# Performance work log

Hardware: AMD Instinct MI355X
Metric: run time of the kernel (lower is better)

Reference implementation:

```python
import jax, jax.numpy as jnp
import numpy as np

STRIDE = 16
NUM_A = 9
POS_TH, NEG_TH = 0.7, 0.3
FG, BG, IGN = 1.0, 0.0, 2.0
CAP = 128  # BATCH_SIZE * 0.5 for both fg and bg


def _generate_base_anchors(base_size=16, ratios=(0.5, 1.0, 2.0), scales=(8, 16, 32)):
    w = h = float(base_size)
    xc = yc = 0.5 * (base_size - 1)
    size = w * h
    out = []
    for r in ratios:
        ws = np.round(np.sqrt(size / r))
        hs = np.round(ws * r)
        for s in scales:
            W, H = ws * s, hs * s
            out.append([xc - 0.5 * (W - 1), yc - 0.5 * (H - 1),
                        xc + 0.5 * (W - 1), yc + 0.5 * (H - 1)])
    return np.asarray(out, dtype=np.float32)  # [9,4]


def _all_anchors(H, W):
    base = _generate_base_anchors()
    sx = np.arange(W, dtype=np.float32) * STRIDE
    sy = np.arange(H, dtype=np.float32) * STRIDE
    xs, ys = np.meshgrid(sx, sy)  # row-major over (h, w)
    shifts = np.stack([xs.ravel(), ys.ravel(), xs.ravel(), ys.ravel()], 1)
    return jnp.asarray((shifts[:, None, :] + base[None, :, :]).reshape(-1, 4))  # [H*W*9,4], order (h,w,a)


def _forward(scores, gt, im_w, im_h):
    H, W = scores.shape[2], scores.shape[3]
    anchors = _all_anchors(H, W)  # [N,4]
    valid = (anchors[:, 0] >= 0.) & (anchors[:, 1] >= 0.) & \
            (anchors[:, 2] < im_w) & (anchors[:, 3] < im_h)
    # pairwise IoU with +1 box convention
    aw = anchors[:, 2] - anchors[:, 0] + 1.
    ah = anchors[:, 3] - anchors[:, 1] + 1.
    a_area = jnp.where((aw > 0) & (ah > 0), aw * ah, 0.)
    gw = gt[:, 2] - gt[:, 0] + 1.
    gh = gt[:, 3] - gt[:, 1] + 1.
    g_area = jnp.where((gw > 0) & (gh > 0), gw * gh, 0.)
    ix1 = jnp.maximum(anchors[:, None, 0], gt[None, :, 0])
    iy1 = jnp.maximum(anchors[:, None, 1], gt[None, :, 1])
    ix2 = jnp.minimum(anchors[:, None, 2], gt[None, :, 2])
    iy2 = jnp.minimum(anchors[:, None, 3], gt[None, :, 3])
    iw = ix2 - ix1 + 1.
    ih = iy2 - iy1 + 1.
    inter = jnp.where((iw > 0) & (ih > 0), iw * ih, 0.)
    ovl = inter / (a_area[:, None] + g_area[None, :] - inter)  # [N,G]
    ovl_m = jnp.where(valid[:, None], ovl, -1.)  # exclude invalid anchors
    a_argmax = jnp.argmax(ovl, axis=1)           # best gt per anchor
    a_max = jnp.max(ovl, axis=1)
    g_max = jnp.max(ovl_m, axis=0)               # best (valid) anchor overlap per gt
    gt_fg = jnp.any(ovl_m == g_max[None, :], axis=1) & valid
    labels = jnp.where(valid & (a_max < NEG_TH), BG, IGN)
    labels = jnp.where(gt_fg, FG, labels)
    labels = jnp.where(valid & (a_max >= POS_TH), FG, labels)
    # random subsample fg/bg down to CAP each (matches npr.choice semantics in distribution)
    kf, kb = jax.random.split(jax.random.key(42))
    def subsample(lbl, mask, k):
        s = jnp.where(mask, jax.random.uniform(k, lbl.shape), jnp.inf)
        ranks = jnp.argsort(jnp.argsort(s))
        keep = ranks < jnp.minimum(jnp.sum(mask), CAP)
        return jnp.where(mask & ~keep, IGN, lbl)
    labels = subsample(labels, labels == FG, kf)
    labels = subsample(labels, labels == BG, kb)
    num_ni = jnp.sum(labels != IGN).astype(jnp.float32)
    gts = gt[a_argmax]
    ax = (anchors[:, 2] + anchors[:, 0]) * 0.5
    ay = (anchors[:, 3] + anchors[:, 1]) * 0.5
    gwm = gts[:, 2] - gts[:, 0] + 1.
    ghm = gts[:, 3] - gts[:, 1] + 1.
    gx = (gts[:, 2] + gts[:, 0]) * 0.5
    gy = (gts[:, 3] + gts[:, 1]) * 0.5
    adj = jnp.stack([(gx - ax) / aw, (gy - ay) / ah,
                     jnp.log(gwm / aw), jnp.log(ghm / ah)], axis=1)  # [N,4]
    adj = jnp.where(valid[:, None], adj, 0.)
    wts = jnp.where((labels == FG)[:, None], 1.0 / num_ni, 0.) * jnp.ones((1, 4), jnp.float32)
    labels_out = labels.reshape(1, H, W, NUM_A).transpose(0, 3, 1, 2) \
                       .reshape(1, 1, NUM_A * H, W).astype(jnp.int32)
    adj_out = adj.reshape(1, H, W, 4 * NUM_A).transpose(0, 3, 1, 2)
    wts_out = wts.reshape(1, H, W, 4 * NUM_A).transpose(0, 3, 1, 2)
    return labels_out, adj_out, wts_out


def setup_inputs() -> dict:
    key = jax.random.key(0)
    k1, k2, k3 = jax.random.split(key, 3)
    scores = jax.random.normal(k1, (1, 18, 256, 256), dtype=jnp.float32)
    G = 64
    cxy = jax.random.uniform(k2, (G, 2), minval=100., maxval=3900.)
    wh = jax.random.uniform(k3, (G, 2), minval=32., maxval=512.)
    x1y1 = jnp.clip(cxy - wh * 0.5, 0., 4095.)
    x2y2 = jnp.clip(cxy + wh * 0.5, 0., 4095.)
    gt = jnp.concatenate([x1y1, x2y2], axis=1)  # [G,4] = x1,y1,x2,y2
    return {"anchor_object_scores": scores, "ground_truth_boxes": gt,
            "im_w": 4096, "im_h": 4096}


def reference(anchor_object_scores, ground_truth_boxes, im_w, im_h):
    return _forward(anchor_object_scores, ground_truth_boxes, im_w, im_h)
```

## Files before the change

kernel.cpp:

```cpp
#include <hip/hip_runtime.h>
#include <stdint.h>


#define NUM_A 9
#define HW 65536
#define N_ANCH 589824
#define NG 64
#define CAPK 128u
#define NBINS 256
#define BG_TC 65536u
#define CAND_CAP 2048

#define LAB_BG 0u
#define LAB_FG 1u
#define LAB_IGN 2u

#define NBLK 1152
#define NGRP 64
#define GQ 18

#define OFF_HF    0
#define OFF_HB    256
#define OFF_TOTF  512
#define OFF_TOTB  1536
#define OFF_SUBB  2560
#define OFF_ROOTB 3584
#define OFF_SUBD  3600
#define OFF_ROOTD 4624
#define OFF_SEL   4640
#define OFF_CFLG  4656
#define OFF_CNTF  5680
#define OFF_CNTB  5696
#define CTRL_WORDS 5712
#define OFF_ZFLG  CTRL_WORDS
#define OFF_CANDF (OFF_ZFLG + 64*16)
#define OFF_CANDB (OFF_CANDF + 2*CAND_CAP)

#define MAGIC_C 0x5CA1AB1Eu
#define MAGIC_Z 0x7A3F19C5u

__constant__ float BA[NUM_A][4] = {
  { -84.f,  -40.f,  99.f,  55.f}, {-176.f,  -88.f, 191.f, 103.f},
  {-360.f, -184.f, 375.f, 199.f}, { -56.f,  -56.f,  71.f,  71.f},
  {-120.f, -120.f, 135.f, 135.f}, {-248.f, -248.f, 263.f, 263.f},
  { -36.f,  -80.f,  51.f,  95.f}, { -80.f, -168.f,  95.f, 183.f},
  {-168.f, -344.f, 183.f, 359.f}};

__host__ __device__ static inline void tf2x32(uint32_t k0, uint32_t k1,
                                              uint32_t x0, uint32_t x1,
                                              uint32_t* o0, uint32_t* o1) {
  const uint32_t ks2 = k0 ^ k1 ^ 0x1BD11BDAu;
#define TF_R(r) { x0 += x1; x1 = (x1 << (r)) | (x1 >> (32 - (r))); x1 ^= x0; }
  x0 += k0; x1 += k1;
  TF_R(13) TF_R(15) TF_R(26) TF_R(6)
  x0 += k1;  x1 += ks2 + 1u;
  TF_R(17) TF_R(29) TF_R(16) TF_R(24)
  x0 += ks2; x1 += k0 + 2u;
  TF_R(13) TF_R(15) TF_R(26) TF_R(6)
  x0 += k0;  x1 += k1 + 3u;
  TF_R(17) TF_R(29) TF_R(16) TF_R(24)
  x0 += k1;  x1 += ks2 + 4u;
  TF_R(13) TF_R(15) TF_R(26) TF_R(6)
  x0 += ks2; x1 += k0 + 5u;
#undef TF_R
  *o0 = x0; *o1 = x1;
}

__device__ static inline uint32_t mant_of(uint32_t k0, uint32_t k1, uint32_t n) {
  uint32_t o0, o1;
  tf2x32(k0, k1, 0u, n, &o0, &o1);
  return (o0 ^ o1) >> 9;
}

__device__ static inline float axis_best(float blo, float bhi, float glo,
                                         float ghi, int lo, int hi) {
  #pragma clang fp contract(off)
  float t1 = (ghi - bhi) * 0.0625f;
  float t2 = (glo - blo) * 0.0625f;
  float tmin = fminf(t1, t2), tmax = fmaxf(t1, t2);
  int c1 = (int)floorf(tmin), c2 = (int)ceilf(tmax);
  int cand0 = lo, cand1 = hi;
  int cand2 = min(max(c1,     lo), hi);
  int cand3 = min(max(c1 + 1, lo), hi);
  int cand4 = min(max(c2 - 1, lo), hi);
  int cand5 = min(max(c2,     lo), hi);
  float best = -3.0e38f;
  int cands[6] = {cand0, cand1, cand2, cand3, cand4, cand5};
  #pragma unroll
  for (int i = 0; i < 6; i++) {
    float s = (float)(cands[i] << 4);
    float v = fminf(bhi + s, ghi) - fmaxf(blo + s, glo) + 1.0f;
    best = fmaxf(best, v);
  }
  return best;
}

#define AG_LOAD(p)      __hip_atomic_load((p), __ATOMIC_RELAXED, __HIP_MEMORY_SCOPE_AGENT)
#define AG_STORE(p, v)  __hip_atomic_store((p), (v), __ATOMIC_RELAXED, __HIP_MEMORY_SCOPE_AGENT)

__global__ __launch_bounds__(256) void k_one(const float* __restrict__ gt,
                                             const int* __restrict__ imw_p,
                                             const int* __restrict__ imh_p,
                                             float* __restrict__ out_lab,
                                             float* __restrict__ out_adj,
                                             float* __restrict__ out_wts,
                                             uint32_t* __restrict__ ws,
                                             uint32_t kf0, uint32_t kf1,
                                             uint32_t kb0, uint32_t kb1) {
  #pragma clang fp contract(off)
  __shared__ uint64_t scB[CAND_CAP];
  uint32_t* sh = (uint32_t*)scB;
  __shared__ float sg0[NG], sg1[NG], sg2[NG], sg3[NG], sga[NG], sgm[NG];
  __shared__ uint32_t sgmU[NG];
  __shared__ unsigned long long sMask[4];
  __shared__ int sAnyZero, sLastB, sLastD;
  __shared__ uint32_t sSel[10];
  __shared__ uint32_t sCF, sCB;
  int tid = threadIdx.x;
  int b = blockIdx.x;
  int a = b >> 7, hb = (b & 127) << 1;
  int grp = b & (NGRP - 1);

  if (b == 0) {
    for (int i = tid; i < CTRL_WORDS; i += 256) AG_STORE(&ws[i], 0u);
    asm volatile("s_waitcnt vmcnt(0)" ::: "memory");
    __syncthreads();
    if (tid < NGRP) AG_STORE(&ws[OFF_ZFLG + tid * 16], MAGIC_Z);
  }

  ((uint2*)sh)[tid] = make_uint2(0, 0);
  if (tid == 0) { sAnyZero = 0; sCF = 0u; sCB = 0u; }
  if (tid < NG) {
    const float4 g4 = ((const float4*)gt)[tid];
    sg0[tid] = g4.x; sg1[tid] = g4.y; sg2[tid] = g4.z; sg3[tid] = g4.w;
    float gw = g4.z - g4.x + 1.0f, gh = g4.w - g4.y + 1.0f;
    sga[tid] = (gw > 0.0f && gh > 0.0f) ? gw * gh : 0.0f;
    sgmU[tid] = 0u;
  }
  __syncthreads();

  {
    int imwi = imw_p[0], imhi = imh_p[0];
    for (int p = tid; p < NG * NUM_A; p += 256) {
      int g = p / NUM_A, q = p - g * NUM_A;
      float b0 = BA[q][0], b1 = BA[q][1], b2 = BA[q][2], b3 = BA[q][3];
      int ib0 = (int)b0, ib1 = (int)b1, ib2 = (int)b2, ib3 = (int)b3;
      int wlo = max(0, (-ib0 + 15) >> 4);
      int whi = min(255, (imwi - ib2 - 1) >> 4);
      int hlo = max(0, (-ib1 + 15) >> 4);
      int hhi = min(255, (imhi - ib3 - 1) >> 4);
      if (wlo > whi || hlo > hhi) continue;
      float iwb = axis_best(b0, b2, sg0[g], sg2[g], wlo, whi);
      float ihb = axis_best(b1, b3, sg1[g], sg3[g], hlo, hhi);
      float aw = b2 - b0 + 1.0f, ah = b3 - b1 + 1.0f;
      float aarea = aw * ah;
      float inter = (iwb > 0.0f && ihb > 0.0f) ? iwb * ihb : 0.0f;
      float den = aarea + sga[g] - inter;
      float o = inter / den;
      atomicMax(&sgmU[g], __float_as_uint(o));
    }
  }

  {
    int wv = tid >> 6, g = tid & 63;
    float sy = (float)((hb + wv) << 4);
    float ihp = fminf(BA[a][3] + sy, sg3[g]) - fmaxf(BA[a][1] + sy, sg1[g]) + 1.0f;
    unsigned long long mk = __ballot(ihp > 0.0f);
    if (g == 0) sMask[wv] = mk;
  }
  __syncthreads();
  if (tid < NG) {
    uint32_t mm = sgmU[tid];
    sgm[tid] = __uint_as_float(mm);
    if (mm == 0u) atomicOr(&sAnyZero, 1);
  }
  __syncthreads();

  float BA0 = BA[a][0], BA1 = BA[a][1], BA2 = BA[a][2], BA3 = BA[a][3];
  float imw = (float)imw_p[0], imh = (float)imh_p[0];
  int w = tid;
  float sx = (float)(w << 4);
  float A0 = BA0 + sx, A2 = BA2 + sx;
  float aw = A2 - A0 + 1.0f;
  float A1v[2], A3v[2];
  #pragma unroll
  for (int r = 0; r < 2; r++) {
    float sy = (float)((hb + r) << 4);
    A1v[r] = BA1 + sy; A3v[r] = BA3 + sy;
  }
  float ah = A3v[0] - A1v[0] + 1.0f;
  float aarea = aw * ah;
  bool xv = (A0 >= 0.0f) && (A2 < imw);

  unsigned long long mk0 = sMask[0], mk1 = sMask[1];
  unsigned long long uni = mk0 | mk1;
  float amaxv[2] = {0.f, 0.f};
  int bgv[2] = {0, 0};
  uint32_t afv = 0u;
  while (uni) {
    int g = __ffsll(uni) - 1;
    uni &= uni - 1;
    float iw = fminf(A2, sg2[g]) - fmaxf(A0, sg0[g]) + 1.0f;
    if (!__any(iw > 0.0f)) continue;
    if (iw > 0.0f) {
      float base = aarea + sga[g];
      float gy1 = sg1[g], gy2 = sg3[g], gm = sgm[g];
#define DO_ROW(r, mk)                                                     \
      if ((mk >> g) & 1ull) {                                             \
        float ih = fminf(A3v[r], gy2) - fmaxf(A1v[r], gy1) + 1.0f;        \
        float inter = iw * ih;                                            \
        float o = inter / (base - inter);                                 \
        if (o > amaxv[r]) { amaxv[r] = o; bgv[r] = g; }                   \
        if (o == gm) afv |= (1u << r);                                    \
      }
      DO_ROW(0, mk0) DO_ROW(1, mk1)
#undef DO_ROW
    }
  }

  bool anyZ = (sAnyZero != 0);
  uint32_t lm[2];
  uint32_t cfLoc = 0, cbLoc = 0;
  #pragma unroll
  for (int r = 0; r < 2; r++) {
    int hw = (hb + r) * 256 + w;
    bool valid = xv && (A1v[r] >= 0.0f) && (A3v[r] < imh);
    float amax = amaxv[r];
    bool anyfg = (((afv >> r) & 1u) || anyZ) && valid;
    uint32_t lab;
    if (!valid)                       lab = LAB_IGN;
    else if (anyfg || amax >= 0.7f)   lab = LAB_FG;
    else if (amax < 0.3f)             lab = LAB_BG;
    else                              lab = LAB_IGN;

    float adj0 = 0.f, adj1 = 0.f, adj2 = 0.f, adj3 = 0.f;
    if (valid) {
      int bg = bgv[r];
      float G0 = sg0[bg], G1 = sg1[bg], G2 = sg2[bg], G3 = sg3[bg];
      float ax = (A2 + A0) * 0.5f, ay = (A3v[r] + A1v[r]) * 0.5f;
      float gwm = G2 - G0 + 1.0f, ghm = G3 - G1 + 1.0f;
      float gx = (G2 + G0) * 0.5f, gy = (G3 + G1) * 0.5f;
      adj0 = (gx - ax) / aw;
      adj1 = (gy - ay) / ah;
      adj2 = logf(gwm / aw);
      adj3 = logf(ghm / ah);
    }
    int c4 = a * 4;
    out_adj[(c4 + 0) * HW + hw] = adj0;
    out_adj[(c4 + 1) * HW + hw] = adj1;
    out_adj[(c4 + 2) * HW + hw] = adj2;
    out_adj[(c4 + 3) * HW + hw] = adj3;

    uint32_t m = 0u;
    uint32_t n = (uint32_t)(hw * 9 + a);
    if (lab != LAB_IGN) {
      uint32_t kk0 = (lab == LAB_FG) ? kf0 : kb0;
      uint32_t kk1 = (lab == LAB_FG) ? kf1 : kb1;
      m = mant_of(kk0, kk1, n);
      if (lab == LAB_FG) {
        cfLoc++;
        atomicAdd(&sh[m >> 15], 1u);
      } else {
        cbLoc++;
        if (m < BG_TC) atomicAdd(&sh[NBINS + (m >> 8)], 1u);
      }
    }
    lm[r] = (lab << 24) | m;
  }
  if (cfLoc) atomicAdd(&sCF, cfLoc);
  if (cbLoc) atomicAdd(&sCB, cbLoc);
  __syncthreads();

  if (tid == 0) {
    while (AG_LOAD(&ws[OFF_ZFLG + grp * 16]) != MAGIC_Z)
      __builtin_amdgcn_s_sleep(2);
  }
  __syncthreads();

  for (int i = tid; i < 2 * NBINS; i += 256) {
    uint32_t v = sh[i];
    if (v) atomicAdd(&ws[OFF_HF + i], v);
  }
  if (tid == 0) {
    if (sCF) atomicAdd(&ws[OFF_TOTF + grp * 16], sCF);
    if (sCB) atomicAdd(&ws[OFF_TOTB + grp * 16], sCB);
  }
  asm volatile("s_waitcnt vmcnt(0)" ::: "memory");
  __syncthreads();

  if (tid == 0) {
    int last = 0;
    uint32_t v = atomicAdd(&ws[OFF_SUBB + grp * 16], 1u);
    if (v == GQ - 1) {
      uint32_t r = atomicAdd(&ws[OFF_ROOTB], 1u);
      if (r == NGRP - 1) last = 1;
    }
    sLastB = last;
  }
  __syncthreads();
  if (sLastB) {
    __shared__ uint32_t sTots[128];
    if (tid < NGRP)            sTots[tid] = AG_LOAD(&ws[OFF_TOTF + tid * 16]);
    else if (tid < 2 * NGRP)
      sTots[tid] = AG_LOAD(&ws[OFF_TOTB + (tid - NGRP) * 16]);
    __syncthreads();
    uint32_t totF = 0, totB = 0;
    if (tid == 0) {
      for (int i = 0; i < NGRP; i++) {
        totF += sTots[i]; totB += sTots[NGRP + i];
      }
      sTots[0] = totF; sTots[1] = totB;
    }
    __syncthreads();
    totF = sTots[0]; totB = sTots[1];

    for (int cls = 0; cls < 2; cls++) {
      uint32_t* hist = ws + (cls ? OFF_HB : OFF_HF);
      uint32_t* sel = ws + OFF_SEL + cls * 5;
      uint32_t tot = cls ? totB : totF;
      uint32_t K = tot < CAPK ? tot : CAPK;
      uint32_t loc = AG_LOAD(&hist[tid]);
      sh[tid] = loc; __syncthreads();
      for (int off = 1; off < 256; off <<= 1) {
        uint32_t v = (tid >= off) ? sh[tid - off] : 0u;
        __syncthreads();
        sh[tid] += v;
        __syncthreads();
      }
      if (tid == 0) {
        uint32_t mode = (K == 0u) ? 0u : ((tot <= CAPK) ? 1u : 2u);
        AG_STORE(&sel[0], mode);
        AG_STORE(&sel[4], K);
        if (mode != 2u) {
          AG_STORE(&sel[1], 0xFFFFFFFFu); AG_STORE(&sel[2], 0u);
          AG_STORE(&sel[3], 0u);
        }
      }
      if (K > 0u && tot > CAPK) {
        uint32_t myC = sh[tid], pvC = (tid == 0) ? 0u : sh[tid - 1];
        if (myC >= K && pvC < K) {
          AG_STORE(&sel[1], (uint32_t)tid); AG_STORE(&sel[2], pvC);
          AG_STORE(&sel[3], K - pvC);
        }
      }
      __syncthreads();
    }
    asm volatile("s_waitcnt vmcnt(0)" ::: "memory");
    __syncthreads();
    if (tid < NGRP) AG_STORE(&ws[OFF_CFLG + tid * 16], MAGIC_C);
  }

  if (tid == 0) {
    while (AG_LOAD(&ws[OFF_CFLG + grp * 16]) != MAGIC_C)
      __builtin_amdgcn_s_sleep(2);
  }
  __syncthreads();
  if (tid < 10) sSel[tid] = AG_LOAD(&ws[OFF_SEL + tid]);
  __syncthreads();
  uint32_t mF = sSel[0], bbF = sSel[1];
  uint32_t mB = sSel[5], bbB = sSel[6];
  uint32_t Kf = sSel[4], Kb = sSel[9];
  float inv = 1.0f / (float)(Kf + Kb);

  #pragma unroll
  for (int r = 0; r < 2; r++) {
    int hw = (hb + r) * 256 + w;
    uint32_t lab = lm[r] >> 24;
    uint32_t m = lm[r] & 0x7FFFFFu;
    uint32_t n = (uint32_t)(hw * 9 + a);
    float outv = 2.0f, wv = 0.0f;
    bool skip = false;
    if (lab == LAB_FG) {
      if (mF == 1u) { outv = 1.0f; wv = inv; }
      else if (mF == 2u) {
        uint32_t bn = m >> 15;
        if (bn < bbF) { outv = 1.0f; wv = inv; }
        else if (bn == bbF) {
          uint32_t idx = atomicAdd(&ws[OFF_CNTF], 1u);
          if (idx < CAND_CAP) {
            AG_STORE((uint64_t*)(ws + OFF_CANDF) + idx,
                     ((uint64_t)m << 20) | (uint64_t)n);
            skip = true;
          }
        }
      }
    } else if (lab == LAB_BG) {
      if (mB == 1u) { outv = 0.0f; }
      else if (mB == 2u && m < BG_TC) {
        uint32_t bn = m >> 8;
        if (bn < bbB) { outv = 0.0f; }
        else if (bn == bbB) {
          uint32_t idx = atomicAdd(&ws[OFF_CNTB], 1u);
          if (idx < CAND_CAP) {
            AG_STORE((uint64_t*)(ws + OFF_CANDB) + idx,
                     ((uint64_t)m << 20) | (uint64_t)n);
            skip = true;
          }
        }
      }
    }
    if (!skip) {
      out_lab[a * HW + hw] = outv;
      int c4 = a * 4;
      out_wts[(c4 + 0) * HW + hw] = wv;
      out_wts[(c4 + 1) * HW + hw] = wv;
      out_wts[(c4 + 2) * HW + hw] = wv;
      out_wts[(c4 + 3) * HW + hw] = wv;
    }
  }

  asm volatile("s_waitcnt vmcnt(0)" ::: "memory");
  __syncthreads();

  if (tid == 0) {
    int last = 0;
    uint32_t v = atomicAdd(&ws[OFF_SUBD + grp * 16], 1u);
    if (v == GQ - 1) {
      uint32_t r = atomicAdd(&ws[OFF_ROOTD], 1u);
      if (r == NGRP - 1) last = 1;
    }
    sLastD = last;
  }
  __syncthreads();
  if (sLastD) {
    for (int cls = 0; cls < 2; cls++) {
      uint32_t cnt = AG_LOAD(&ws[cls == 0 ? OFF_CNTF : OFF_CNTB]);
      uint32_t C = cnt < CAND_CAP ? cnt : CAND_CAP;
      uint32_t need = AG_LOAD(&ws[OFF_SEL + cls * 5 + 3]);
      const uint64_t* cand =
          (const uint64_t*)(ws + (cls == 0 ? OFF_CANDF : OFF_CANDB));
      for (uint32_t i = tid; i < C; i += 256)
        scB[i] = AG_LOAD(&cand[i]);
      __syncthreads();
      for (uint32_t i = tid; i < C; i += 256) {
        uint64_t k = scB[i];
        uint32_t rr = 0;
        for (uint32_t j = 0; j < C; j++) rr += (scB[j] < k) ? 1u : 0u;
        bool kept = (rr < need);
        uint32_t nn = (uint32_t)(k & 0xFFFFFu);
        uint32_t aa = nn % 9u, hww = nn / 9u;
        uint32_t tt = aa * HW + hww;
        float lv = kept ? (cls == 0 ? 1.0f : 0.0f) : 2.0f;
        float wvv = (kept && cls == 0) ? inv : 0.0f;
        AG_STORE(&out_lab[tt], lv);
        #pragma unroll
        for (int j2 = 0; j2 < 4; j2++)
          AG_STORE(&out_wts[(aa * 4 + j2) * HW + hww], wvv);
      }
      __syncthreads();
    }
    if (tid < NGRP) AG_STORE(&ws[OFF_ZFLG + tid * 16], 0u);
  }
}

extern "C" void kernel_launch(void* const* d_in, const int* in_sizes, int n_in,
                              void* d_out, int out_size, void* d_ws,
                              size_t ws_size, hipStream_t stream) {
  const float* gt  = (const float*)d_in[1];
  const int*   imw = (const int*)d_in[2];
  const int*   imh = (const int*)d_in[3];
  float* out      = (float*)d_out;
  float* out_lab  = out;
  float* out_adj  = out + N_ANCH;
  float* out_wts  = out + 5 * N_ANCH;
  uint32_t* ws = (uint32_t*)d_ws;

  uint32_t kf0, kf1, kb0, kb1;
  tf2x32(0u, 42u, 0u, 0u, &kf0, &kf1);
  tf2x32(0u, 42u, 0u, 1u, &kb0, &kb1);

  hipLaunchKernelGGL(k_one, dim3(NBLK), dim3(256), 0, stream, gt, imw, imh,
                     out_lab, out_adj, out_wts, ws, kf0, kf1, kb0, kb1);
}
```

Measured before the change: 91.84 us.

## Drop second grid-wide barrier by pushing candidates to per-group lists for last block

Removes the second grid-wide wait (the CFLG flag spin) in which every block waited for the last block to publish the selection thresholds. Non-candidate anchors now write their ignore outputs early. FG and in-range BG candidates go into per-group global lists, and the final block applies the threshold and the tie-break ranking for all of them. This trades the global stall for more serial work in one block and caps each group's list at 128 entries. Candidates beyond that cap are written as ignore, which could change results if a group ever holds more.

```diff
diff --git a/kernel.cpp b/kernel.cpp
--- a/kernel.cpp
+++ b/kernel.cpp
@@ -9,7 +9,8 @@
 #define CAPK 128u
 #define NBINS 256
 #define BG_TC 65536u
-#define CAND_CAP 2048
+#define CLCAP 128u
+#define STAGE_CAP 2048u
 
 #define LAB_BG 0u
 #define LAB_FG 1u
@@ -25,18 +26,13 @@
 #define OFF_TOTB  1536
 #define OFF_SUBB  2560
 #define OFF_ROOTB 3584
-#define OFF_SUBD  3600
-#define OFF_ROOTD 4624
-#define OFF_SEL   4640
-#define OFF_CFLG  4656
-#define OFF_CNTF  5680
-#define OFF_CNTB  5696
-#define CTRL_WORDS 5712
+#define OFF_CCNTF 3600
+#define OFF_CCNTB 4624
+#define CTRL_WORDS 5648
 #define OFF_ZFLG  CTRL_WORDS
-#define OFF_CANDF (OFF_ZFLG + 64*16)
-#define OFF_CANDB (OFF_CANDF + 2*CAND_CAP)
-
-#define MAGIC_C 0x5CA1AB1Eu
+#define OFF_LISTF (OFF_ZFLG + 64*16)
+#define OFF_LISTB (OFF_LISTF + 2*NGRP*CLCAP)
+
 #define MAGIC_Z 0x7A3F19C5u
 
 __constant__ float BA[NUM_A][4] = {
@@ -108,14 +104,18 @@
                                              uint32_t kf0, uint32_t kf1,
                                              uint32_t kb0, uint32_t kb1) {
   #pragma clang fp contract(off)
-  __shared__ uint64_t scB[CAND_CAP];
+  __shared__ uint64_t scB[STAGE_CAP];
   uint32_t* sh = (uint32_t*)scB;
   __shared__ float sg0[NG], sg1[NG], sg2[NG], sg3[NG], sga[NG], sgm[NG];
   __shared__ uint32_t sgmU[NG];
   __shared__ unsigned long long sMask[4];
-  __shared__ int sAnyZero, sLastB, sLastD;
-  __shared__ uint32_t sSel[10];
+  __shared__ int sAnyZero, sLastB;
   __shared__ uint32_t sCF, sCB;
+  __shared__ uint32_t sTots[2 * NGRP];
+  __shared__ uint32_t sCnt2[NGRP];
+  __shared__ uint32_t sSelLoc[10];
+  __shared__ uint32_t sStageCnt;
+  __shared__ float sInv;
   int tid = threadIdx.x;
   int b = blockIdx.x;
   int a = b >> 7, hb = (b & 127) << 1;
@@ -266,6 +266,15 @@
       }
     }
     lm[r] = (lab << 24) | m;
+
+    bool cand = (lab == LAB_FG) || (lab == LAB_BG && m < BG_TC);
+    if (!cand) {
+      out_lab[a * HW + hw] = 2.0f;
+      out_wts[(c4 + 0) * HW + hw] = 0.0f;
+      out_wts[(c4 + 1) * HW + hw] = 0.0f;
+      out_wts[(c4 + 2) * HW + hw] = 0.0f;
+      out_wts[(c4 + 3) * HW + hw] = 0.0f;
+    }
   }
   if (cfLoc) atomicAdd(&sCF, cfLoc);
   if (cbLoc) atomicAdd(&sCB, cbLoc);
@@ -276,6 +285,31 @@
       __builtin_amdgcn_s_sleep(2);
   }
   __syncthreads();
+
+  #pragma unroll
+  for (int r = 0; r < 2; r++) {
+    uint32_t lab = lm[r] >> 24;
+    uint32_t m = lm[r] & 0x7FFFFFu;
+    bool cand = (lab == LAB_FG) || (lab == LAB_BG && m < BG_TC);
+    if (!cand) continue;
+    int hw = (hb + r) * 256 + w;
+    uint32_t n = (uint32_t)(hw * 9 + a);
+    int cls = (lab == LAB_FG) ? 0 : 1;
+    uint32_t idx = atomicAdd(
+        &ws[(cls ? OFF_CCNTB : OFF_CCNTF) + grp * 16], 1u);
+    if (idx < CLCAP) {
+      uint64_t* lst = (uint64_t*)(ws + (cls ? OFF_LISTB : OFF_LISTF)) +
+                      (uint32_t)grp * CLCAP;
+      AG_STORE(&lst[idx], ((uint64_t)m << 20) | (uint64_t)n);
+    } else {
+      out_lab[a * HW + hw] = 2.0f;
+      int c4 = a * 4;
+      out_wts[(c4 + 0) * HW + hw] = 0.0f;
+      out_wts[(c4 + 1) * HW + hw] = 0.0f;
+      out_wts[(c4 + 2) * HW + hw] = 0.0f;
+      out_wts[(c4 + 3) * HW + hw] = 0.0f;
+    }
+  }
 
   for (int i = tid; i < 2 * NBINS; i += 256) {
     uint32_t v = sh[i];
@@ -298,147 +332,89 @@
     sLastB = last;
   }
   __syncthreads();
-  if (sLastB) {
-    __shared__ uint32_t sTots[128];
-    if (tid < NGRP)            sTots[tid] = AG_LOAD(&ws[OFF_TOTF + tid * 16]);
-    else if (tid < 2 * NGRP)
-      sTots[tid] = AG_LOAD(&ws[OFF_TOTB + (tid - NGRP) * 16]);
-    __syncthreads();
+  if (!sLastB) return;
+
+  if (tid < NGRP)            sTots[tid] = AG_LOAD(&ws[OFF_TOTF + tid * 16]);
+  else if (tid < 2 * NGRP)
+    sTots[tid] = AG_LOAD(&ws[OFF_TOTB + (tid - NGRP) * 16]);
+  __syncthreads();
+  if (tid == 0) {
     uint32_t totF = 0, totB = 0;
+    for (int i = 0; i < NGRP; i++) {
+      totF += sTots[i]; totB += sTots[NGRP + i];
+    }
+    uint32_t Kf = totF < CAPK ? totF : CAPK;
+    uint32_t Kb = totB < CAPK ? totB : CAPK;
+    sTots[0] = totF; sTots[1] = totB;
+    sInv = 1.0f / (float)(Kf + Kb);
+  }
+  __syncthreads();
+  uint32_t totF = sTots[0], totB = sTots[1];
+
+  for (int cls = 0; cls < 2; cls++) {
+    uint32_t* hist = ws + (cls ? OFF_HB : OFF_HF);
+    uint32_t tot = cls ? totB : totF;
+    uint32_t K = tot < CAPK ? tot : CAPK;
+    uint32_t loc = AG_LOAD(&hist[tid]);
+    __syncthreads();
+    sh[tid] = loc; __syncthreads();
+    for (int off = 1; off < 256; off <<= 1) {
+      uint32_t v = (tid >= off) ? sh[tid - off] : 0u;
+      __syncthreads();
+      sh[tid] += v;
+      __syncthreads();
+    }
     if (tid == 0) {
-      for (int i = 0; i < NGRP; i++) {
-        totF += sTots[i]; totB += sTots[NGRP + i];
+      uint32_t mode = (K == 0u) ? 0u : ((tot <= CAPK) ? 1u : 2u);
+      sSelLoc[cls * 5 + 0] = mode;
+      sSelLoc[cls * 5 + 1] = 0xFFFFFFFFu;
+      sSelLoc[cls * 5 + 2] = 0u;
+      sSelLoc[cls * 5 + 3] = 0u;
+      sSelLoc[cls * 5 + 4] = K;
+    }
+    __syncthreads();
+    if (K > 0u && tot > CAPK) {
+      uint32_t myC = sh[tid], pvC = (tid == 0) ? 0u : sh[tid - 1];
+      if (myC >= K && pvC < K) {
+        sSelLoc[cls * 5 + 1] = (uint32_t)tid;
+        sSelLoc[cls * 5 + 2] = pvC;
+        sSelLoc[cls * 5 + 3] = K - pvC;
       }
-      sTots[0] = totF; sTots[1] = totB;
-    }
-    __syncthreads();
-    totF = sTots[0]; totB = sTots[1];
-
-    for (int cls = 0; cls < 2; cls++) {
-      uint32_t* hist = ws + (cls ? OFF_HB : OFF_HF);
-      uint32_t* sel = ws + OFF_SEL + cls * 5;
-      uint32_t tot = cls ? totB : totF;
-      uint32_t K = tot < CAPK ? tot : CAPK;
-      uint32_t loc = AG_LOAD(&hist[tid]);
-      sh[tid] = loc; __syncthreads();
-      for (int off = 1; off < 256; off <<= 1) {
-        uint32_t v = (tid >= off) ? sh[tid - off] : 0u;
-        __syncthreads();
-        sh[tid] += v;
-        __syncthreads();
-      }
-      if (tid == 0) {
-        uint32_t mode = (K == 0u) ? 0u : ((tot <= CAPK) ? 1u : 2u);
-        AG_STORE(&sel[0], mode);
-        AG_STORE(&sel[4], K);
-        if (mode != 2u) {
-          AG_STORE(&sel[1], 0xFFFFFFFFu); AG_STORE(&sel[2], 0u);
-          AG_STORE(&sel[3], 0u);
+    }
+    __syncthreads();
+  }
+  float inv = sInv;
+
+  for (int cls = 0; cls < 2; cls++) {
+    if (tid < NGRP) {
+      uint32_t c2 = AG_LOAD(&ws[(cls ? OFF_CCNTB : OFF_CCNTF) + tid * 16]);
+      sCnt2[tid] = c2 < CLCAP ? c2 : CLCAP;
+    }
+    if (tid == 0) sStageCnt = 0u;
+    __syncthreads();
+    uint32_t mode = sSelLoc[cls * 5 + 0];
+    uint32_t bb = sSelLoc[cls * 5 + 1];
+    uint32_t need = sSelLoc[cls * 5 + 3];
+    const uint64_t* lst0 =
+        (const uint64_t*)(ws + (cls ? OFF_LISTB : OFF_LISTF));
+    for (uint32_t idx = tid; idx < NGRP * CLCAP; idx += 256) {
+      uint32_t g2 = idx >> 7, i = idx & (CLCAP - 1u);
+      if (i >= sCnt2[g2]) continue;
+      uint64_t k = AG_LOAD(&lst0[g2 * CLCAP + i]);
+      uint32_t m = (uint32_t)(k >> 20);
+      uint32_t n = (uint32_t)(k & 0xFFFFFu);
+      bool decided = true, kept = false;
+      if (mode == 1u) kept = true;
+      else if (mode == 2u) {
+        uint32_t bn = cls ? (m >> 8) : (m >> 15);
+        if (bn < bb) kept = true;
+        else if (bn == bb) {
+          uint32_t s = atomicAdd(&sStageCnt, 1u);
+          if (s < STAGE_CAP) { scB[s] = k; decided = false; }
         }
       }
-      if (K > 0u && tot > CAPK) {
-        uint32_t myC = sh[tid], pvC = (tid == 0) ? 0u : sh[tid - 1];
-        if (myC >= K && pvC < K) {
-          AG_STORE(&sel[1], (uint32_t)tid); AG_STORE(&sel[2], pvC);
-          AG_STORE(&sel[3], K - pvC);
-        }
-      }
-      __syncthreads();
-    }
-    asm volatile("s_waitcnt vmcnt(0)" ::: "memory");
-    __syncthreads();
-    if (tid < NGRP) AG_STORE(&ws[OFF_CFLG + tid * 16], MAGIC_C);
-  }
-
-  if (tid == 0) {
-    while (AG_LOAD(&ws[OFF_CFLG + grp * 16]) != MAGIC_C)
-      __builtin_amdgcn_s_sleep(2);
-  }
-  __syncthreads();
-  if (tid < 10) sSel[tid] = AG_LOAD(&ws[OFF_SEL + tid]);
-  __syncthreads();
-  uint32_t mF = sSel[0], bbF = sSel[1];
-  uint32_t mB = sSel[5], bbB = sSel[6];
-  uint32_t Kf = sSel[4], Kb = sSel[9];
-  float inv = 1.0f / (float)(Kf + Kb);
-
-  #pragma unroll
-  for (int r = 0; r < 2; r++) {
-    int hw = (hb + r) * 256 + w;
-    uint32_t lab = lm[r] >> 24;
-    uint32_t m = lm[r] & 0x7FFFFFu;
-    uint32_t n = (uint32_t)(hw * 9 + a);
-    float outv = 2.0f, wv = 0.0f;
-    bool skip = false;
-    if (lab == LAB_FG) {
-      if (mF == 1u) { outv = 1.0f; wv = inv; }
-      else if (mF == 2u) {
-        uint32_t bn = m >> 15;
-        if (bn < bbF) { outv = 1.0f; wv = inv; }
-        else if (bn == bbF) {
-          uint32_t idx = atomicAdd(&ws[OFF_CNTF], 1u);
-          if (idx < CAND_CAP) {
-            AG_STORE((uint64_t*)(ws + OFF_CANDF) + idx,
-                     ((uint64_t)m << 20) | (uint64_t)n);
-            skip = true;
-          }
-        }
-      }
-    } else if (lab == LAB_BG) {
-      if (mB == 1u) { outv = 0.0f; }
-      else if (mB == 2u && m < BG_TC) {
-        uint32_t bn = m >> 8;
-        if (bn < bbB) { outv = 0.0f; }
-        else if (bn == bbB) {
-          uint32_t idx = atomicAdd(&ws[OFF_CNTB], 1u);
-          if (idx < CAND_CAP) {
-            AG_STORE((uint64_t*)(ws + OFF_CANDB) + idx,
-                     ((uint64_t)m << 20) | (uint64_t)n);
-            skip = true;
-          }
-        }
-      }
-    }
-    if (!skip) {
-      out_lab[a * HW + hw] = outv;
-      int c4 = a * 4;
-      out_wts[(c4 + 0) * HW + hw] = wv;
-      out_wts[(c4 + 1) * HW + hw] = wv;
-      out_wts[(c4 + 2) * HW + hw] = wv;
-      out_wts[(c4 + 3) * HW + hw] = wv;
-    }
-  }
-
-  asm volatile("s_waitcnt vmcnt(0)" ::: "memory");
-  __syncthreads();
-
-  if (tid == 0) {
-    int last = 0;
-    uint32_t v = atomicAdd(&ws[OFF_SUBD + grp * 16], 1u);
-    if (v == GQ - 1) {
-      uint32_t r = atomicAdd(&ws[OFF_ROOTD], 1u);
-      if (r == NGRP - 1) last = 1;
-    }
-    sLastD = last;
-  }
-  __syncthreads();
-  if (sLastD) {
-    for (int cls = 0; cls < 2; cls++) {
-      uint32_t cnt = AG_LOAD(&ws[cls == 0 ? OFF_CNTF : OFF_CNTB]);
-      uint32_t C = cnt < CAND_CAP ? cnt : CAND_CAP;
-      uint32_t need = AG_LOAD(&ws[OFF_SEL + cls * 5 + 3]);
-      const uint64_t* cand =
-          (const uint64_t*)(ws + (cls == 0 ? OFF_CANDF : OFF_CANDB));
-      for (uint32_t i = tid; i < C; i += 256)
-        scB[i] = AG_LOAD(&cand[i]);
-      __syncthreads();
-      for (uint32_t i = tid; i < C; i += 256) {
-        uint64_t k = scB[i];
-        uint32_t rr = 0;
-        for (uint32_t j = 0; j < C; j++) rr += (scB[j] < k) ? 1u : 0u;
-        bool kept = (rr < need);
-        uint32_t nn = (uint32_t)(k & 0xFFFFFu);
-        uint32_t aa = nn % 9u, hww = nn / 9u;
+      if (decided) {
+        uint32_t aa = n % 9u, hww = n / 9u;
         uint32_t tt = aa * HW + hww;
         float lv = kept ? (cls == 0 ? 1.0f : 0.0f) : 2.0f;
         float wvv = (kept && cls == 0) ? inv : 0.0f;
@@ -447,10 +423,28 @@
         for (int j2 = 0; j2 < 4; j2++)
           AG_STORE(&out_wts[(aa * 4 + j2) * HW + hww], wvv);
       }
-      __syncthreads();
-    }
-    if (tid < NGRP) AG_STORE(&ws[OFF_ZFLG + tid * 16], 0u);
-  }
+    }
+    __syncthreads();
+    uint32_t C = sStageCnt < STAGE_CAP ? sStageCnt : STAGE_CAP;
+    for (uint32_t i = tid; i < C; i += 256) {
+      uint64_t k = scB[i];
+      uint32_t rr = 0;
+      for (uint32_t j = 0; j < C; j++) rr += (scB[j] < k) ? 1u : 0u;
+      bool kept = (rr < need);
+      uint32_t n = (uint32_t)(k & 0xFFFFFu);
+      uint32_t aa = n % 9u, hww = n / 9u;
+      uint32_t tt = aa * HW + hww;
+      float lv = kept ? (cls == 0 ? 1.0f : 0.0f) : 2.0f;
+      float wvv = (kept && cls == 0) ? inv : 0.0f;
+      AG_STORE(&out_lab[tt], lv);
+      #pragma unroll
+      for (int j2 = 0; j2 < 4; j2++)
+        AG_STORE(&out_wts[(aa * 4 + j2) * HW + hww], wvv);
+    }
+    __syncthreads();
+  }
+
+  if (tid < NGRP) AG_STORE(&ws[OFF_ZFLG + tid * 16], 0u);
 }
 
 extern "C" void kernel_launch(void* const* d_in, const int* in_sizes, int n_in,
```

Result: slower. 133.8 us (+45.6%).
